# Performance work log

Measured on AMD Instinct MI355X. Metric: run time of the kernel, lower is better.

The kernel has to match this reference:

```python
import jax, jax.numpy as jnp
import numpy as np

H = 16  # num_heads
ROPE_BASE = 10000.0

def _rotate_half(x):
    d = x.shape[-1]
    return jnp.concatenate((-x[..., d // 2:], x[..., :d // 2]), axis=-1)

def setup_inputs() -> dict:
    key = jax.random.key(0)
    ks = jax.random.split(key, 9)
    B, S, E = 4, 2048, 1024
    s = 0.02
    return {
        "x": jax.random.normal(ks[0], (B, S, E), dtype=jnp.float32),
        "wq": jax.random.normal(ks[1], (E, E), dtype=jnp.float32) * s,
        "bq": jax.random.normal(ks[2], (E,), dtype=jnp.float32) * s,
        "wk": jax.random.normal(ks[3], (E, E), dtype=jnp.float32) * s,
        "bk": jax.random.normal(ks[4], (E,), dtype=jnp.float32) * s,
        "wv": jax.random.normal(ks[5], (E, E), dtype=jnp.float32) * s,
        "bv": jax.random.normal(ks[6], (E,), dtype=jnp.float32) * s,
        "wo": jax.random.normal(ks[7], (E, E), dtype=jnp.float32) * s,
        "bo": jax.random.normal(ks[8], (E,), dtype=jnp.float32) * s,
    }

def reference(x, wq, bq, wk, bk, wv, bv, wo, bo):
    B, S, E = x.shape
    D = E // H  # head_dim
    # projections (nn.Linear: x @ W.T + b), then split heads -> (B, H, S, D)
    def proj(w, b):
        return (x @ w.T + b).reshape(B, S, H, D).transpose(0, 2, 1, 3)
    q = proj(wq, bq)
    k = proj(wk, bk)
    v = proj(wv, bv)
    # RoPE: freqs (S, D//2) -> repeat_interleave(2) -> (S, D)
    inv_freq = 1.0 / (ROPE_BASE ** (jnp.arange(0, D, 2, dtype=jnp.float32) / D))
    freqs = jnp.arange(S, dtype=jnp.float32)[:, None] * inv_freq[None, :]
    cos = jnp.repeat(jnp.cos(freqs), 2, axis=-1)[None, None]  # (1,1,S,D)
    sin = jnp.repeat(jnp.sin(freqs), 2, axis=-1)[None, None]
    q = q * cos + _rotate_half(q) * sin
    k = k * cos + _rotate_half(k) * sin
    scale = D ** (-0.5)
    scores = jnp.einsum('bhqd,bhkd->bhqk', q, k) * scale
    attn = jax.nn.softmax(scores, axis=-1)
    out = jnp.einsum('bhqk,bhkd->bhqd', attn, v)  # (B,H,S,D)
    out = out.transpose(0, 2, 1, 3).reshape(B, S, E)
    return out @ wo.T + bo
```

## Files before the change

### kernel.cpp

```cpp
#include <hip/hip_runtime.h>


typedef __attribute__((ext_vector_type(4))) float f32x4;
typedef __attribute__((ext_vector_type(8))) short bfrag;
typedef __attribute__((ext_vector_type(4))) short svec4;
typedef __attribute__((ext_vector_type(2))) unsigned int u32x2;

#define MFMA16(a, b, c) __builtin_amdgcn_mfma_f32_16x16x32_bf16(a, b, c, 0, 0, 0)

__device__ __forceinline__ unsigned short f2bf(float f) {
  unsigned u = __builtin_bit_cast(unsigned, f);
  u += 0x7FFFu + ((u >> 16) & 1u);
  return (unsigned short)(u >> 16);
}

__device__ __forceinline__ void gload16(const void* g, void* l) {
  __builtin_amdgcn_global_load_lds(
      (const __attribute__((address_space(1))) unsigned int*)g,
      (__attribute__((address_space(3))) unsigned int*)l, 16, 0, 0);
}

__global__ __launch_bounds__(256) void prep_kernel(
    const float* __restrict__ x, const float* __restrict__ wq,
    const float* __restrict__ wk, const float* __restrict__ wv,
    const float* __restrict__ wo,
    unsigned short* __restrict__ xb, unsigned short* __restrict__ wqb,
    unsigned short* __restrict__ wkb, unsigned short* __restrict__ wvb,
    unsigned short* __restrict__ wob, float2* __restrict__ rope) {
  const int y = blockIdx.y;
  const int tid = blockIdx.x * blockDim.x + threadIdx.x;
  const int stride = gridDim.x * blockDim.x;
  if (y < 5) {
    const float* src = y == 0 ? x : y == 1 ? wq : y == 2 ? wk : y == 3 ? wv : wo;
    unsigned short* dst = y == 0 ? xb : y == 1 ? wqb : y == 2 ? wkb : y == 3 ? wvb : wob;
    const int n4 = (y == 0 ? (8192 * 1024) : (1024 * 1024)) >> 2;
    for (int i = tid; i < n4; i += stride) {
      float4 v = ((const float4*)src)[i];
      svec4 o;
      o.x = (short)f2bf(v.x); o.y = (short)f2bf(v.y);
      o.z = (short)f2bf(v.z); o.w = (short)f2bf(v.w);
      ((svec4*)dst)[i] = o;
    }
  } else {
    for (int i = tid; i < 2048 * 32; i += stride) {
      int s = i >> 5, f = i & 31;
      float invf = powf(10000.0f, -(float)f * (1.0f / 32.0f));
      float ang = (float)s * invf;
      rope[i] = make_float2(cosf(ang), sinf(ang));
    }
  }
}

__global__ __launch_bounds__(256) void gemm_qkv(
    const unsigned short* __restrict__ Xb,
    const unsigned short* __restrict__ Wq, const unsigned short* __restrict__ Wk,
    const unsigned short* __restrict__ Wv,
    const float* __restrict__ biasq, const float* __restrict__ biask,
    const float* __restrict__ biasv,
    const float2* __restrict__ rope,
    unsigned short* __restrict__ Qo, unsigned short* __restrict__ Ko,
    unsigned short* __restrict__ Vto) {
  const int z = blockIdx.z;
  __shared__ unsigned short As[128 * 64];
  __shared__ unsigned short Bs[128 * 64];
  const int t = threadIdx.x;
  const int lane = t & 63, w = t >> 6;
  const int wr = w >> 1, wc = w & 1;
  const int lc = lane & 15, lr = lane >> 4;

  int m0, n0;
  const unsigned short *Apt, *Bpt;
  if (z == 0)      { m0 = blockIdx.y * 128; n0 = blockIdx.x * 128; Apt = Xb; Bpt = Wq; }
  else if (z == 1) { m0 = blockIdx.y * 128; n0 = blockIdx.x * 128; Apt = Xb; Bpt = Wk; }
  else             { m0 = blockIdx.x * 128; n0 = blockIdx.y * 128; Apt = Wv; Bpt = Xb; }

  const int arow = t >> 3;
  const int acol = ((t & 7) << 3) ^ ((arow & 7) << 3);
  const unsigned short* gA = Apt + (size_t)(m0 + arow) * 1024 + acol;
  const unsigned short* gB = Bpt + (size_t)(n0 + arow) * 1024 + acol;
  unsigned short* lA = As + t * 8;
  unsigned short* lB = Bs + t * 8;

  f32x4 acc[4][4];
#pragma unroll
  for (int m = 0; m < 4; ++m)
#pragma unroll
    for (int n = 0; n < 4; ++n) acc[m][n] = (f32x4){0.f, 0.f, 0.f, 0.f};

  const int rsw = (lc & 7) << 3;

#pragma unroll 1
  for (int kt = 0; kt < 16; ++kt) {
    __syncthreads();
#pragma unroll
    for (int c = 0; c < 4; ++c) {
      gload16(gA + (size_t)c * 32 * 1024, lA + c * 2048);
      gload16(gB + (size_t)c * 32 * 1024, lB + c * 2048);
    }
    gA += 64; gB += 64;
    __syncthreads();
#pragma unroll
    for (int ks = 0; ks < 2; ++ks) {
      bfrag af[4], bfr[4];
#pragma unroll
      for (int i = 0; i < 4; ++i)
        af[i] = *(const bfrag*)(As + (wr * 64 + i * 16 + lc) * 64 + ((ks * 32 + lr * 8) ^ rsw));
#pragma unroll
      for (int i = 0; i < 4; ++i)
        bfr[i] = *(const bfrag*)(Bs + (wc * 64 + i * 16 + lc) * 64 + ((ks * 32 + lr * 8) ^ rsw));
#pragma unroll
      for (int m = 0; m < 4; ++m)
#pragma unroll
        for (int n = 0; n < 4; ++n)
          acc[m][n] = MFMA16(af[m], bfr[n], acc[m][n]);
    }
  }

  if (z < 2) {
    const float* bias = (z == 0) ? biasq : biask;
    unsigned short* dst = (z == 0) ? Qo : Ko;
    const float qs = (z == 0) ? 0.125f * 1.44269504f : 1.0f;
    const int h = (n0 + wc * 64) >> 6;
#pragma unroll
    for (int m = 0; m < 4; ++m) {
#pragma unroll
      for (int r = 0; r < 4; ++r) {
        int row = m0 + wr * 64 + m * 16 + lr * 4 + r;
        int b = row >> 11, s = row & 2047;
        const float2* trow = rope + (s << 5);
        size_t base = ((size_t)((b << 4) + h) * 2048 + s) * 64;
#pragma unroll
        for (int n = 0; n < 2; ++n) {
          int col1 = n0 + wc * 64 + n * 16 + lc;
          int d = n * 16 + lc;
          float a  = acc[m][n][r]     + bias[col1];
          float bb = acc[m][n + 2][r] + bias[col1 + 32];
          float2 t0 = trow[d >> 1];
          float2 t1 = trow[16 + (d >> 1)];
          dst[base + d]      = f2bf((a * t0.x - bb * t0.y) * qs);
          dst[base + d + 32] = f2bf((bb * t1.x + a * t1.y) * qs);
        }
      }
    }
  } else {
#pragma unroll
    for (int m = 0; m < 4; ++m) {
#pragma unroll
      for (int r = 0; r < 4; ++r) {
        int wcol = m0 + wr * 64 + m * 16 + lr * 4 + r;
        float bv = biasv[wcol];
        int h = wcol >> 6, d = wcol & 63;
#pragma unroll
        for (int n = 0; n < 4; ++n) {
          int token = n0 + wc * 64 + n * 16 + lc;
          int b = token >> 11, s = token & 2047;
          Vto[((size_t)((b << 4) + h) * 64 + d) * 2048 + s] = f2bf(acc[m][n][r] + bv);
        }
      }
    }
  }
}

__global__ __launch_bounds__(256) void attn_kernel(
    const unsigned short* __restrict__ Q, const unsigned short* __restrict__ K,
    const unsigned short* __restrict__ Vt, unsigned short* __restrict__ O) {
  __shared__ unsigned short Ks[2][64 * 64];
  __shared__ unsigned short Vs[2][64 * 64];
  __shared__ unsigned short Plds[4][16 * 64];
  const int t = threadIdx.x;
  const int lane = t & 63, w = t >> 6;
  const int lc = lane & 15, lr = lane >> 4;
  const int bid = blockIdx.x;
  const int xcd = bid & 7;
  const int jj = bid >> 3;
  const int bh = xcd * 8 + (jj >> 5);
  const int qb = jj & 31;
  const int q0 = qb * 64 + w * 16;

  const unsigned short* Qp = Q + ((size_t)bh * 2048 + q0 + lc) * 64 + lr * 8;
  bfrag aq0 = *(const bfrag*)Qp;
  bfrag aq1 = *(const bfrag*)(Qp + 32);

  f32x4 acc[4];
#pragma unroll
  for (int n = 0; n < 4; ++n) acc[n] = (f32x4){0.f, 0.f, 0.f, 0.f};
  float lsum = 0.f;

  const unsigned short* Kg = K + (size_t)bh * 2048 * 64;
  const unsigned short* Vg = Vt + (size_t)bh * 64 * 2048;

  unsigned short* Pw = &Plds[w][0];
  const int swz = lc & 7;
  unsigned short* pws = Pw + lc * 64 + 4 * (lr & 1);
  const int rsw = swz << 3;

  const int srow = t >> 3;
  const int scol = ((t & 7) ^ (srow & 7)) << 3;

#define STAGE(bufi, kb_)                                                        \
  {                                                                             \
    gload16(Kg + (size_t)((kb_) + srow) * 64 + scol,        Ks[bufi] + t * 8);  \
    gload16(Kg + (size_t)((kb_) + 32 + srow) * 64 + scol,   Ks[bufi] + 2048 + t * 8); \
    gload16(Vg + (size_t)srow * 2048 + (kb_) + scol,        Vs[bufi] + t * 8);  \
    gload16(Vg + (size_t)(32 + srow) * 2048 + (kb_) + scol, Vs[bufi] + 2048 + t * 8); \
  }

  STAGE(0, 0);
  STAGE(1, 64);
  int cur = 0;

#pragma unroll 1
  for (int kt = 0; kt < 32; ++kt) {
    if (kt < 30) { asm volatile("s_waitcnt vmcnt(4)" ::: "memory"); }
    else         { asm volatile("s_waitcnt vmcnt(0)" ::: "memory"); }
    __builtin_amdgcn_s_barrier();

    const unsigned short* KsC = Ks[cur];
    const unsigned short* VsC = Vs[cur];

    f32x4 sc[4];
    __builtin_amdgcn_s_setprio(1);
#pragma unroll
    for (int c = 0; c < 4; ++c) {
      const unsigned short* kp = KsC + (c * 16 + lc) * 64;
      bfrag k0 = *(const bfrag*)(kp + ((lr * 8) ^ rsw));
      bfrag k1 = *(const bfrag*)(kp + ((32 + lr * 8) ^ rsw));
      f32x4 z = (f32x4){0.f, 0.f, 0.f, 0.f};
      z = MFMA16(k0, aq0, z);
      sc[c] = MFMA16(k1, aq1, z);
    }
    __builtin_amdgcn_s_setprio(0);

#pragma unroll
    for (int c = 0; c < 4; ++c)
#pragma unroll
      for (int r = 0; r < 4; ++r)
        sc[c][r] = __builtin_amdgcn_exp2f(sc[c][r]);
    {
      float s0 = (sc[0][0] + sc[0][1]) + (sc[0][2] + sc[0][3]);
      float s1 = (sc[1][0] + sc[1][1]) + (sc[1][2] + sc[1][3]);
      float s2 = (sc[2][0] + sc[2][1]) + (sc[2][2] + sc[2][3]);
      float s3 = (sc[3][0] + sc[3][1]) + (sc[3][2] + sc[3][3]);
      lsum += (s0 + s1) + (s2 + s3);
    }

#pragma unroll
    for (int c = 0; c < 4; ++c) {
      unsigned pk0, pk1;
      asm("v_cvt_pk_bf16_f32 %0, %1, %2" : "=v"(pk0) : "v"(sc[c][0]), "v"(sc[c][1]));
      asm("v_cvt_pk_bf16_f32 %0, %1, %2" : "=v"(pk1) : "v"(sc[c][2]), "v"(sc[c][3]));
      u32x2 pk; pk.x = pk0; pk.y = pk1;
      *(u32x2*)(pws + (((2 * c + (lr >> 1)) ^ swz) << 3)) = pk;
    }

    bfrag ap0 = *(const bfrag*)(Pw + lc * 64 + ((lr ^ swz) << 3));
    bfrag ap1 = *(const bfrag*)(Pw + lc * 64 + (((4 + lr) ^ swz) << 3));

    __builtin_amdgcn_s_setprio(1);
#pragma unroll
    for (int n = 0; n < 4; ++n) {
      const unsigned short* vp = VsC + (n * 16 + lc) * 64;
      bfrag bv0 = *(const bfrag*)(vp + ((lr * 8) ^ rsw));
      bfrag bv1 = *(const bfrag*)(vp + ((32 + lr * 8) ^ rsw));
      acc[n] = MFMA16(ap0, bv0, acc[n]);
      acc[n] = MFMA16(ap1, bv1, acc[n]);
    }
    __builtin_amdgcn_s_setprio(0);

    __builtin_amdgcn_s_barrier();
    if (kt + 2 < 32) STAGE(cur, (kt + 2) * 64);
    cur ^= 1;
  }
#undef STAGE

  float v = lsum;
  v += __shfl_xor(v, 16);
  v += __shfl_xor(v, 32);
  float inv[4];
#pragma unroll
  for (int r = 0; r < 4; ++r)
    inv[r] = 1.0f / __shfl(v, lr * 4 + r);

  const int b = bh >> 4, h = bh & 15;
#pragma unroll
  for (int r = 0; r < 4; ++r) {
    int s = q0 + lr * 4 + r;
    size_t base = (((size_t)b * 2048 + s) * 16 + h) * 64;
#pragma unroll
    for (int n = 0; n < 4; ++n)
      O[base + n * 16 + lc] = f2bf(acc[n][r] * inv[r]);
  }
}

__global__ __launch_bounds__(256) void gemm_out(
    const unsigned short* __restrict__ Ob, const unsigned short* __restrict__ Wo,
    const float* __restrict__ bias, float* __restrict__ out) {
  __shared__ unsigned short As[128 * 64];
  __shared__ unsigned short Bs[128 * 64];
  const int t = threadIdx.x;
  const int lane = t & 63, w = t >> 6;
  const int wr = w >> 1, wc = w & 1;
  const int lc = lane & 15, lr = lane >> 4;
  const int m0 = blockIdx.y * 128, n0 = blockIdx.x * 128;

  const int arow = t >> 3;
  const int acol = ((t & 7) << 3) ^ ((arow & 7) << 3);
  const unsigned short* gA = Ob + (size_t)(m0 + arow) * 1024 + acol;
  const unsigned short* gB = Wo + (size_t)(n0 + arow) * 1024 + acol;
  unsigned short* lA = As + t * 8;
  unsigned short* lB = Bs + t * 8;

  f32x4 acc[4][4];
#pragma unroll
  for (int m = 0; m < 4; ++m)
#pragma unroll
    for (int n = 0; n < 4; ++n) acc[m][n] = (f32x4){0.f, 0.f, 0.f, 0.f};

  const int rsw = (lc & 7) << 3;

#pragma unroll 1
  for (int kt = 0; kt < 16; ++kt) {
    __syncthreads();
#pragma unroll
    for (int c = 0; c < 4; ++c) {
      gload16(gA + (size_t)c * 32 * 1024, lA + c * 2048);
      gload16(gB + (size_t)c * 32 * 1024, lB + c * 2048);
    }
    gA += 64; gB += 64;
    __syncthreads();
#pragma unroll
    for (int ks = 0; ks < 2; ++ks) {
      bfrag af[4], bfr[4];
#pragma unroll
      for (int i = 0; i < 4; ++i)
        af[i] = *(const bfrag*)(As + (wr * 64 + i * 16 + lc) * 64 + ((ks * 32 + lr * 8) ^ rsw));
#pragma unroll
      for (int i = 0; i < 4; ++i)
        bfr[i] = *(const bfrag*)(Bs + (wc * 64 + i * 16 + lc) * 64 + ((ks * 32 + lr * 8) ^ rsw));
#pragma unroll
      for (int m = 0; m < 4; ++m)
#pragma unroll
        for (int n = 0; n < 4; ++n)
          acc[m][n] = MFMA16(af[m], bfr[n], acc[m][n]);
    }
  }
#pragma unroll
  for (int n = 0; n < 4; ++n) {
    int col = n0 + wc * 64 + n * 16 + lc;
    float bv = bias[col];
#pragma unroll
    for (int m = 0; m < 4; ++m) {
#pragma unroll
      for (int r = 0; r < 4; ++r) {
        int row = m0 + wr * 64 + m * 16 + lr * 4 + r;
        out[(size_t)row * 1024 + col] = acc[m][n][r] + bv;
      }
    }
  }
}

extern "C" void kernel_launch(void* const* d_in, const int* in_sizes, int n_in,
                              void* d_out, int out_size, void* d_ws, size_t ws_size,
                              hipStream_t stream) {
  (void)in_sizes; (void)n_in; (void)out_size; (void)ws_size;
  const float* x  = (const float*)d_in[0];
  const float* wq = (const float*)d_in[1];
  const float* bq = (const float*)d_in[2];
  const float* wk = (const float*)d_in[3];
  const float* bk = (const float*)d_in[4];
  const float* wv = (const float*)d_in[5];
  const float* bv = (const float*)d_in[6];
  const float* wo = (const float*)d_in[7];
  const float* bo = (const float*)d_in[8];
  float* out = (float*)d_out;

  char* ws = (char*)d_ws;
  unsigned short* Xb   = (unsigned short*)(ws);
  unsigned short* Wqb  = (unsigned short*)(ws + (16ull << 20));
  unsigned short* Wkb  = (unsigned short*)(ws + (18ull << 20));
  unsigned short* Wvb  = (unsigned short*)(ws + (20ull << 20));
  unsigned short* Wob  = (unsigned short*)(ws + (22ull << 20));
  unsigned short* Qb   = (unsigned short*)(ws + (24ull << 20));
  unsigned short* Kb   = (unsigned short*)(ws + (40ull << 20));
  unsigned short* Vt   = (unsigned short*)(ws + (56ull << 20));
  float2* rope         = (float2*)(ws + (72ull << 20));
  unsigned short* Ob   = Xb;

  prep_kernel<<<dim3(1024, 6), 256, 0, stream>>>(x, wq, wk, wv, wo,
                                                 Xb, Wqb, Wkb, Wvb, Wob, rope);
  gemm_qkv<<<dim3(8, 64, 3), 256, 0, stream>>>(Xb, Wqb, Wkb, Wvb,
                                               bq, bk, bv, rope, Qb, Kb, Vt);
  attn_kernel<<<2048, 256, 0, stream>>>(Qb, Kb, Vt, Ob);
  gemm_out<<<dim3(8, 64), 256, 0, stream>>>(Ob, Wob, bo, out);
}
```

Baseline: 221.5 us.

## Switch attention to 32x32 MFMA tiles with register-shuffled P instead of LDS

Rewrites the attention inner loop to use 32x32x16 bf16 MFMAs, with each wave handling 32 query rows and each block 128 rows, so the grid is halved. The probability tile is repacked into A-operand layout with cross-half-wave shuffles rather than a round trip through shared memory, which removes the P LDS buffer and its writes and reads. Each K/V tile staged in LDS is reused across twice as many queries. The cost is more accumulator registers per wave (two 16-float outputs plus scores) and fewer blocks, which may lower occupancy.

```diff
diff --git a/kernel.cpp b/kernel.cpp
--- a/kernel.cpp
+++ b/kernel.cpp
@@ -2,11 +2,13 @@
 
 
 typedef __attribute__((ext_vector_type(4))) float f32x4;
+typedef __attribute__((ext_vector_type(16))) float f32x16;
 typedef __attribute__((ext_vector_type(8))) short bfrag;
 typedef __attribute__((ext_vector_type(4))) short svec4;
-typedef __attribute__((ext_vector_type(2))) unsigned int u32x2;
+typedef __attribute__((ext_vector_type(4))) unsigned u32x4;
 
 #define MFMA16(a, b, c) __builtin_amdgcn_mfma_f32_16x16x32_bf16(a, b, c, 0, 0, 0)
+#define MFMA32(a, b, c) __builtin_amdgcn_mfma_f32_32x32x16_bf16(a, b, c, 0, 0, 0)
 
 __device__ __forceinline__ unsigned short f2bf(float f) {
   unsigned u = __builtin_bit_cast(unsigned, f);
@@ -166,33 +168,30 @@
     const unsigned short* __restrict__ Vt, unsigned short* __restrict__ O) {
   __shared__ unsigned short Ks[2][64 * 64];
   __shared__ unsigned short Vs[2][64 * 64];
-  __shared__ unsigned short Plds[4][16 * 64];
   const int t = threadIdx.x;
   const int lane = t & 63, w = t >> 6;
-  const int lc = lane & 15, lr = lane >> 4;
+  const int l31 = lane & 31, th = lane >> 5;
   const int bid = blockIdx.x;
   const int xcd = bid & 7;
   const int jj = bid >> 3;
-  const int bh = xcd * 8 + (jj >> 5);
-  const int qb = jj & 31;
-  const int q0 = qb * 64 + w * 16;
-
-  const unsigned short* Qp = Q + ((size_t)bh * 2048 + q0 + lc) * 64 + lr * 8;
-  bfrag aq0 = *(const bfrag*)Qp;
-  bfrag aq1 = *(const bfrag*)(Qp + 32);
-
-  f32x4 acc[4];
-#pragma unroll
-  for (int n = 0; n < 4; ++n) acc[n] = (f32x4){0.f, 0.f, 0.f, 0.f};
+  const int bh = xcd * 8 + (jj >> 4);
+  const int qb = jj & 15;
+  const int q0 = qb * 128 + w * 32;
+
+  const unsigned short* Qp = Q + ((size_t)bh * 2048 + q0 + l31) * 64 + th * 8;
+  bfrag bq[4];
+#pragma unroll
+  for (int kk = 0; kk < 4; ++kk) bq[kk] = *(const bfrag*)(Qp + kk * 16);
+
+  f32x16 accO0, accO1;
+#pragma unroll
+  for (int i = 0; i < 16; ++i) { accO0[i] = 0.f; accO1[i] = 0.f; }
   float lsum = 0.f;
 
   const unsigned short* Kg = K + (size_t)bh * 2048 * 64;
   const unsigned short* Vg = Vt + (size_t)bh * 64 * 2048;
 
-  unsigned short* Pw = &Plds[w][0];
-  const int swz = lc & 7;
-  unsigned short* pws = Pw + lc * 64 + 4 * (lr & 1);
-  const int rsw = swz << 3;
+  const int rs = (l31 & 7) << 3;
 
   const int srow = t >> 3;
   const int scol = ((t & 7) ^ (srow & 7)) << 3;
@@ -218,52 +217,66 @@
     const unsigned short* KsC = Ks[cur];
     const unsigned short* VsC = Vs[cur];
 
-    f32x4 sc[4];
+    bfrag pa[4];
+
+#pragma unroll
+    for (int kb = 0; kb < 2; ++kb) {
+      f32x16 sc;
+#pragma unroll
+      for (int i = 0; i < 16; ++i) sc[i] = 0.f;
+      const unsigned short* kp = KsC + (kb * 32 + l31) * 64;
+      __builtin_amdgcn_s_setprio(1);
+#pragma unroll
+      for (int kk = 0; kk < 4; ++kk) {
+        bfrag ka = *(const bfrag*)(kp + ((kk * 16 + th * 8) ^ rs));
+        sc = MFMA32(ka, bq[kk], sc);
+      }
+      __builtin_amdgcn_s_setprio(0);
+
+#pragma unroll
+      for (int i = 0; i < 16; ++i) sc[i] = __builtin_amdgcn_exp2f(sc[i]);
+      {
+        float s0 = (sc[0] + sc[1]) + (sc[2] + sc[3]);
+        float s1 = (sc[4] + sc[5]) + (sc[6] + sc[7]);
+        float s2 = (sc[8] + sc[9]) + (sc[10] + sc[11]);
+        float s3 = (sc[12] + sc[13]) + (sc[14] + sc[15]);
+        lsum += (s0 + s1) + (s2 + s3);
+      }
+
+      unsigned pk[4][2];
+#pragma unroll
+      for (int g = 0; g < 4; ++g) {
+        asm("v_cvt_pk_bf16_f32 %0, %1, %2"
+            : "=v"(pk[g][0]) : "v"(sc[4 * g]), "v"(sc[4 * g + 1]));
+        asm("v_cvt_pk_bf16_f32 %0, %1, %2"
+            : "=v"(pk[g][1]) : "v"(sc[4 * g + 2]), "v"(sc[4 * g + 3]));
+      }
+
+#pragma unroll
+      for (int ka = 0; ka < 2; ++ka) {
+        u32x4 pu;
+#pragma unroll
+        for (int j = 0; j < 2; ++j) {
+          unsigned zlo = pk[2 * ka][j];
+          unsigned zhi = pk[2 * ka + 1][j];
+          unsigned zsend = th ? zlo : zhi;
+          unsigned wv = (unsigned)__shfl_xor((int)zsend, 32);
+          pu[j]     = th ? wv : zlo;
+          pu[2 + j] = th ? zhi : wv;
+        }
+        pa[kb * 2 + ka] = __builtin_bit_cast(bfrag, pu);
+      }
+    }
+
     __builtin_amdgcn_s_setprio(1);
 #pragma unroll
-    for (int c = 0; c < 4; ++c) {
-      const unsigned short* kp = KsC + (c * 16 + lc) * 64;
-      bfrag k0 = *(const bfrag*)(kp + ((lr * 8) ^ rsw));
-      bfrag k1 = *(const bfrag*)(kp + ((32 + lr * 8) ^ rsw));
-      f32x4 z = (f32x4){0.f, 0.f, 0.f, 0.f};
-      z = MFMA16(k0, aq0, z);
-      sc[c] = MFMA16(k1, aq1, z);
-    }
-    __builtin_amdgcn_s_setprio(0);
-
-#pragma unroll
-    for (int c = 0; c < 4; ++c)
-#pragma unroll
-      for (int r = 0; r < 4; ++r)
-        sc[c][r] = __builtin_amdgcn_exp2f(sc[c][r]);
-    {
-      float s0 = (sc[0][0] + sc[0][1]) + (sc[0][2] + sc[0][3]);
-      float s1 = (sc[1][0] + sc[1][1]) + (sc[1][2] + sc[1][3]);
-      float s2 = (sc[2][0] + sc[2][1]) + (sc[2][2] + sc[2][3]);
-      float s3 = (sc[3][0] + sc[3][1]) + (sc[3][2] + sc[3][3]);
-      lsum += (s0 + s1) + (s2 + s3);
-    }
-
-#pragma unroll
-    for (int c = 0; c < 4; ++c) {
-      unsigned pk0, pk1;
-      asm("v_cvt_pk_bf16_f32 %0, %1, %2" : "=v"(pk0) : "v"(sc[c][0]), "v"(sc[c][1]));
-      asm("v_cvt_pk_bf16_f32 %0, %1, %2" : "=v"(pk1) : "v"(sc[c][2]), "v"(sc[c][3]));
-      u32x2 pk; pk.x = pk0; pk.y = pk1;
-      *(u32x2*)(pws + (((2 * c + (lr >> 1)) ^ swz) << 3)) = pk;
-    }
-
-    bfrag ap0 = *(const bfrag*)(Pw + lc * 64 + ((lr ^ swz) << 3));
-    bfrag ap1 = *(const bfrag*)(Pw + lc * 64 + (((4 + lr) ^ swz) << 3));
-
-    __builtin_amdgcn_s_setprio(1);
-#pragma unroll
-    for (int n = 0; n < 4; ++n) {
-      const unsigned short* vp = VsC + (n * 16 + lc) * 64;
-      bfrag bv0 = *(const bfrag*)(vp + ((lr * 8) ^ rsw));
-      bfrag bv1 = *(const bfrag*)(vp + ((32 + lr * 8) ^ rsw));
-      acc[n] = MFMA16(ap0, bv0, acc[n]);
-      acc[n] = MFMA16(ap1, bv1, acc[n]);
+    for (int kg = 0; kg < 4; ++kg) {
+      const unsigned short* vp0 = VsC + (size_t)l31 * 64;
+      const unsigned short* vp1 = VsC + (size_t)(32 + l31) * 64;
+      bfrag vb0 = *(const bfrag*)(vp0 + ((kg * 16 + th * 8) ^ rs));
+      bfrag vb1 = *(const bfrag*)(vp1 + ((kg * 16 + th * 8) ^ rs));
+      accO0 = MFMA32(pa[kg], vb0, accO0);
+      accO1 = MFMA32(pa[kg], vb1, accO1);
     }
     __builtin_amdgcn_s_setprio(0);
 
@@ -273,22 +286,17 @@
   }
 #undef STAGE
 
-  float v = lsum;
-  v += __shfl_xor(v, 16);
-  v += __shfl_xor(v, 32);
-  float inv[4];
-#pragma unroll
-  for (int r = 0; r < 4; ++r)
-    inv[r] = 1.0f / __shfl(v, lr * 4 + r);
+  float v = lsum + __shfl_xor(lsum, 32);
+  float inv = 1.0f / v;
 
   const int b = bh >> 4, h = bh & 15;
 #pragma unroll
-  for (int r = 0; r < 4; ++r) {
-    int s = q0 + lr * 4 + r;
-    size_t base = (((size_t)b * 2048 + s) * 16 + h) * 64;
-#pragma unroll
-    for (int n = 0; n < 4; ++n)
-      O[base + n * 16 + lc] = f2bf(acc[n][r] * inv[r]);
+  for (int r = 0; r < 16; ++r) {
+    int qrow = (r & 3) + 8 * (r >> 2) + 4 * th;
+    float invr = __shfl(inv, qrow);
+    size_t base = (((size_t)b * 2048 + q0 + qrow) * 16 + h) * 64 + l31;
+    O[base]      = f2bf(accO0[r] * invr);
+    O[base + 32] = f2bf(accO1[r] * invr);
   }
 }
 
@@ -390,6 +398,6 @@
                                                  Xb, Wqb, Wkb, Wvb, Wob, rope);
   gemm_qkv<<<dim3(8, 64, 3), 256, 0, stream>>>(Xb, Wqb, Wkb, Wvb,
                                                bq, bk, bv, rope, Qb, Kb, Vt);
-  attn_kernel<<<2048, 256, 0, stream>>>(Qb, Kb, Vt, Ob);
+  attn_kernel<<<1024, 256, 0, stream>>>(Qb, Kb, Vt, Ob);
   gemm_out<<<dim3(8, 64), 256, 0, stream>>>(Ob, Wob, bo, out);
 }
```

Result: no change. 221.6 us (+0.1%).
